# Kernel optimization log

Hardware: AMD Instinct MI355X
Metric: run time of the kernel (lower is better)

Reference implementation:

```python
import jax, jax.numpy as jnp
import numpy as np

N_NODES = 100000
N_EDGES = 1600000
IN_F = 64
HIDDEN = [64, 64, 32]


def _glorot(key, shape):
    limit = float(np.sqrt(6.0 / (shape[0] + shape[1])))
    return jax.random.uniform(key, shape, jnp.float32, -limit, limit)


def setup_inputs() -> dict:
    key = jax.random.key(0)
    ks = jax.random.split(key, 5)
    x = jax.random.normal(ks[0], (N_NODES, IN_F), jnp.float32)
    edge_index = jax.random.randint(ks[1], (2, N_EDGES), 0, N_NODES, jnp.int64)
    dims = [IN_F] + HIDDEN
    params = {}
    for i in range(len(HIDDEN)):
        params[f"W{i+1}"] = _glorot(ks[2 + i], (dims[i], dims[i + 1]))
        params[f"b{i+1}"] = jnp.zeros((dims[i + 1],), jnp.float32)
    return {"x": x, "edge_index": edge_index, **params}


def _gcn_layer(x, src, dst, norm, W, b, n):
    # PyG GCNConv: linear transform, then normalized scatter-sum aggregation, then bias
    h = x @ W                                  # [N, out]
    msg = norm[:, None] * h[src]               # gather + edge scaling, [E+N, out]
    out = jax.ops.segment_sum(msg, dst, num_segments=n)
    return out + b


def reference(x, edge_index, W1, b1, W2, b2, W3, b3):
    n = x.shape[0]
    # add self-loops (GCNConv default add_self_loops=True)
    loops = jnp.arange(n, dtype=edge_index.dtype)
    src = jnp.concatenate([edge_index[0], loops])
    dst = jnp.concatenate([edge_index[1], loops])
    # symmetric normalization: deg over destination (col), norm = d^-1/2[src]*d^-1/2[dst]
    deg = jax.ops.segment_sum(jnp.ones_like(src, x.dtype), dst, num_segments=n)
    dinv = jnp.where(deg > 0, jax.lax.rsqrt(deg), 0.0)
    norm = dinv[src] * dinv[dst]
    h = jax.nn.relu(_gcn_layer(x, src, dst, norm, W1, b1, n))
    h = jax.nn.relu(_gcn_layer(h, src, dst, norm, W2, b2, n))
    return _gcn_layer(h, src, dst, norm, W3, b3, n)
```

## Files before the change

### kernel.cpp

```cpp
#include <hip/hip_runtime.h>
#include <hip/hip_bf16.h>


#define BLOCK 256
#define NBUCKET 512
#define CHUNK 4096
#define SLOT 4608
#define MAX_NPB 256

typedef float f32x4 __attribute__((ext_vector_type(4)));
typedef short bf16x8 __attribute__((ext_vector_type(8)));

__device__ __forceinline__ float4 fma4(float s, float4 a, float4 b) {
  return make_float4(fmaf(s, a.x, b.x), fmaf(s, a.y, b.y),
                     fmaf(s, a.z, b.z), fmaf(s, a.w, b.w));
}

__device__ __forceinline__ unsigned int bf16r(float f) {
  unsigned int u = __float_as_uint(f);
  u += 0x7fffu + ((u >> 16) & 1u);
  return u >> 16;
}

__device__ __forceinline__ void bsplit(float v, unsigned int& h,
                                       unsigned int& l) {
  h = bf16r(v);
  float r = v - __uint_as_float(h << 16);
  l = bf16r(r);
}

__device__ __forceinline__ void acc_bf8(float4& lo, float4& hi, uint4 u) {
  lo.x += __uint_as_float(u.x << 16);
  lo.y += __uint_as_float(u.x & 0xffff0000u);
  lo.z += __uint_as_float(u.y << 16);
  lo.w += __uint_as_float(u.y & 0xffff0000u);
  hi.x += __uint_as_float(u.z << 16);
  hi.y += __uint_as_float(u.z & 0xffff0000u);
  hi.z += __uint_as_float(u.w << 16);
  hi.w += __uint_as_float(u.w & 0xffff0000u);
// ... 45 lines not shown
      binned[b2 * SLOT + base[b2] + o2] = s4.z | ((d4.z - b2 * npb) << 17);
      binned[b3 * SLOT + base[b3] + o3] = s4.w | ((d4.w - b3 * npb) << 17);
    } else {
      for (int t = 0; t < 4; ++t) {
        if (i + t < e) {
          int d = dst[i + t];
          int bkt = d / npb;
          int lofs = atomicAdd(&h[bkt], 1);
          binned[bkt * SLOT + base[bkt] + lofs] =
              src[i + t] | ((d - bkt * npb) << 17);
        }
      }
    }
  }
}

__global__ __launch_bounds__(BLOCK) void bucket_build(
    const int* __restrict__ binned, const int* __restrict__ bcursor,
    int* __restrict__ offs, int* __restrict__ cnt, float* __restrict__ dinv,
    int* __restrict__ csr_src, int n, int npb) {
  __shared__ int nhist[MAX_NPB];
  __shared__ int noff[MAX_NPB];
  __shared__ int lcsr[SLOT];
  const int b = blockIdx.x;
  const int node_base = b * npb;
  const int nodes = min(npb, n - node_base);
  if (nodes <= 0) return;
  const int ebase = b * SLOT;
  const int ecnt = bcursor[b];
  for (int i = threadIdx.x; i < npb; i += BLOCK) nhist[i] = 0;
  __syncthreads();
  for (int i = threadIdx.x; i < ecnt; i += BLOCK)
    atomicAdd(&nhist[binned[ebase + i] >> 17], 1);
  __syncthreads();
  if (threadIdx.x < 64) {
    const int lane = threadIdx.x;
    const int bi = lane * 4;
    int v0 = (bi + 0 < nodes) ? nhist[bi + 0] : 0;
    int v1 = (bi + 1 < nodes) ? nhist[bi + 1] : 0;
    int v2 = (bi + 2 < nodes) ? nhist[bi + 2] : 0;
    int v3 = (bi + 3 < nodes) ? nhist[bi + 3] : 0;
    int tsum = v0 + v1 + v2 + v3;
    int s = tsum;
#pragma unroll
    for (int o = 1; o < 64; o <<= 1) {
      int u = __shfl_up(s, o, 64);
      if (lane >= o) s += u;
    }
    int texcl = s - tsum;
    if (bi + 0 < nodes) noff[bi + 0] = texcl;
    if (bi + 1 < nodes) noff[bi + 1] = texcl + v0;
    if (bi + 2 < nodes) noff[bi + 2] = texcl + v0 + v1;
    if (bi + 3 < nodes) noff[bi + 3] = texcl + v0 + v1 + v2;
  }
  __syncthreads();
  for (int i = threadIdx.x; i < nodes; i += BLOCK) {
    int c = nhist[i];
    offs[node_base + i] = ebase + noff[i];
    cnt[node_base + i] = c;
    dinv[node_base + i] = rsqrtf((float)(c + 1));
  }
  __syncthreads();
  for (int i = threadIdx.x; i < ecnt; i += BLOCK) {
    int v = binned[ebase + i];
    int pos = atomicAdd(&noff[v >> 17], 1);
    lcsr[pos] = v & 0x1ffff;
  }
  __syncthreads();
  for (int i = threadIdx.x; i < ecnt; i += BLOCK)
    csr_src[ebase + i] = lcsr[i];
}

__global__ __launch_bounds__(BLOCK) void wprep_kernel(
    const float* __restrict__ W1, const float* __restrict__ W2,
    const float* __restrict__ W3, unsigned short* __restrict__ Wt) {
  int t = blockIdx.x * BLOCK + threadIdx.x;
  float v;
  int hi_off, lo_off;
  if (t < 4096) {
    int nn = t >> 6, k = t & 63;
    v = W1[k * 64 + nn];
    hi_off = t;
    lo_off = 4096 + t;
  } else if (t < 8192) {
    int i = t - 4096;
    int nn = i >> 6, k = i & 63;
    v = W2[k * 64 + nn];
    hi_off = 8192 + i;
    lo_off = 12288 + i;
  } else {
    int i = t - 8192;
    if (i >= 2048) return;
    int nn = i >> 6, k = i & 63;
    v = W3[k * 32 + nn];
    hi_off = 16384 + i;
    lo_off = 18432 + i;
  }
  unsigned int h, l;
  bsplit(v, h, l);
  Wt[hi_off] = (unsigned short)h;
  Wt[lo_off] = (unsigned short)l;
}


__global__ __launch_bounds__(BLOCK) void gemm1_kernel(
    const float* __restrict__ x, const unsigned short* __restrict__ Wt,
    const float* __restrict__ dinv, unsigned short* __restrict__ hbf, int n) {
  __shared__ unsigned short Ahi[16][72];
  __shared__ unsigned short Alo[16][72];
  __shared__ float dvs[16];
  const int r16 = threadIdx.x >> 4;
  const int c4 = (threadIdx.x & 15) * 4;
  const int node = blockIdx.x * 16 + r16;
  const int wv = threadIdx.x >> 6;
  const int fr = threadIdx.x & 15;
  const int fq = (threadIdx.x >> 4) & 3;
  const unsigned short* wb = Wt + ((wv * 16 + fr) * 64) + fq * 8;
  bf16x8 bh0 = *(const bf16x8*)(wb);
  bf16x8 bh1 = *(const bf16x8*)(wb + 32);
  bf16x8 bl0 = *(const bf16x8*)(wb + 4096);
  bf16x8 bl1 = *(const bf16x8*)(wb + 4096 + 32);
  uint2 ph = make_uint2(0u, 0u), pl = make_uint2(0u, 0u);
  if (node < n) {
    f32x4 xv =
        __builtin_nontemporal_load((const f32x4*)(x + (size_t)node * 64 + c4));
    unsigned int h0, l0, h1, l1, h2, l2, h3, l3;
    bsplit(xv.x, h0, l0);
    bsplit(xv.y, h1, l1);
    bsplit(xv.z, h2, l2);
    bsplit(xv.w, h3, l3);
    ph = make_uint2(h0 | (h1 << 16), h2 | (h3 << 16));
    pl = make_uint2(l0 | (l1 << 16), l2 | (l3 << 16));
  }
  *(uint2*)(&Ahi[r16][c4]) = ph;
  *(uint2*)(&Alo[r16][c4]) = pl;
  if ((threadIdx.x & 15) == 0) dvs[r16] = (node < n) ? dinv[node] : 0.f;
  __syncthreads();
  bf16x8 ah0 = *(const bf16x8*)(&Ahi[fr][fq * 8]);
  bf16x8 ah1 = *(const bf16x8*)(&Ahi[fr][fq * 8 + 32]);
  bf16x8 aL0 = *(const bf16x8*)(&Alo[fr][fq * 8]);
  bf16x8 aL1 = *(const bf16x8*)(&Alo[fr][fq * 8 + 32]);
  f32x4 acc = {0.f, 0.f, 0.f, 0.f};
  acc = __builtin_amdgcn_mfma_f32_16x16x32_bf16(ah0, bh0, acc, 0, 0, 0);
  acc = __builtin_amdgcn_mfma_f32_16x16x32_bf16(aL0, bh0, acc, 0, 0, 0);
  acc = __builtin_amdgcn_mfma_f32_16x16x32_bf16(ah0, bl0, acc, 0, 0, 0);
  acc = __builtin_amdgcn_mfma_f32_16x16x32_bf16(ah1, bh1, acc, 0, 0, 0);
  acc = __builtin_amdgcn_mfma_f32_16x16x32_bf16(aL1, bh1, acc, 0, 0, 0);
  acc = __builtin_amdgcn_mfma_f32_16x16x32_bf16(ah1, bl1, acc, 0, 0, 0);
  const int col = wv * 16 + fr;
#pragma unroll
  for (int j = 0; j < 4; ++j) {
    int row = fq * 4 + j;
    int nd = blockIdx.x * 16 + row;
    if (nd < n)
      hbf[(size_t)nd * 64 + col] = (unsigned short)bf16r(dvs[row] * acc[j]);
  }
}

__global__ __launch_bounds__(BLOCK) void fused_agg_gemm64(
    const unsigned short* __restrict__ hin, const int* __restrict__ csr_src,
    const int* __restrict__ offs, const int* __restrict__ cnt,
    const float* __restrict__ dinv, const float* __restrict__ bias,
    const unsigned short* __restrict__ Wt, unsigned short* __restrict__ hout,
    int n) {
  __shared__ unsigned short Ahi[16][72];
  __shared__ unsigned short Alo[16][72];
  __shared__ float dvs[16];
  const int g = threadIdx.x >> 4;
  const int lane16 = threadIdx.x & 15;
  const int colgrp = lane16 & 7;
  const int half = lane16 >> 3;
  const int c8 = colgrp * 8;
  const int node = blockIdx.x * 16 + g;
  const bool valid = node < n;
  float dnode = 0.f;
  uint4 qh = make_uint4(0u, 0u, 0u, 0u), ql = make_uint4(0u, 0u, 0u, 0u);
  if (valid) {
    const int start = offs[node];
    const int cn = cnt[node];
    const unsigned short* hcol = hin + c8;
    float4 l0 = make_float4(0.f, 0.f, 0.f, 0.f), h0 = l0;
    float4 l1 = l0, h1 = l0, l2 = l0, h2 = l0, l3 = l0, h3 = l0;
    if (half == 0)
      acc_bf8(l0, h0, *(const uint4*)(hcol + (size_t)node * 64));
    int j = half * 4;
    for (; j + 4 <= cn; j += 8) {
      int s0 = csr_src[start + j + 0];
      int s1 = csr_src[start + j + 1];
      int s2 = csr_src[start + j + 2];
      int s3 = csr_src[start + j + 3];
      uint4 u0 = *(const uint4*)(hcol + (size_t)s0 * 64);
      uint4 u1 = *(const uint4*)(hcol + (size_t)s1 * 64);
      uint4 u2 = *(const uint4*)(hcol + (size_t)s2 * 64);
      uint4 u3 = *(const uint4*)(hcol + (size_t)s3 * 64);
      acc_bf8(l0, h0, u0);
      acc_bf8(l1, h1, u1);
      acc_bf8(l2, h2, u2);
      acc_bf8(l3, h3, u3);
    }
    if (j < cn) {
      int rem = cn - j;
      int s0 = csr_src[start + j];
      acc_bf8(l1, h1, *(const uint4*)(hcol + (size_t)s0 * 64));
      if (rem > 1) {
        int s1 = csr_src[start + j + 1];
        acc_bf8(l2, h2, *(const uint4*)(hcol + (size_t)s1 * 64));
      }
      if (rem > 2) {
        int s2 = csr_src[start + j + 2];
        acc_bf8(l3, h3, *(const uint4*)(hcol + (size_t)s2 * 64));
      }
    }
    float4 alo = make_float4((l0.x + l1.x) + (l2.x + l3.x),
                             (l0.y + l1.y) + (l2.y + l3.y),
                             (l0.z + l1.z) + (l2.z + l3.z),
                             (l0.w + l1.w) + (l2.w + l3.w));
    float4 ahi = make_float4((h0.x + h1.x) + (h2.x + h3.x),
                             (h0.y + h1.y) + (h2.y + h3.y),
                             (h0.z + h1.z) + (h2.z + h3.z),
                             (h0.w + h1.w) + (h2.w + h3.w));
    alo.x += __shfl_xor(alo.x, 8); alo.y += __shfl_xor(alo.y, 8);
    alo.z += __shfl_xor(alo.z, 8); alo.w += __shfl_xor(alo.w, 8);
    ahi.x += __shfl_xor(ahi.x, 8); ahi.y += __shfl_xor(ahi.y, 8);
    ahi.z += __shfl_xor(ahi.z, 8); ahi.w += __shfl_xor(ahi.w, 8);
    dnode = dinv[node];
    if (half == 0) {
      float4 b4l = *(const float4*)(bias + c8);
      float4 b4h = *(const float4*)(bias + c8 + 4);
      float v0 = fmaxf(fmaf(dnode, alo.x, b4l.x), 0.f);
      float v1 = fmaxf(fmaf(dnode, alo.y, b4l.y), 0.f);
      float v2 = fmaxf(fmaf(dnode, alo.z, b4l.z), 0.f);
      float v3 = fmaxf(fmaf(dnode, alo.w, b4l.w), 0.f);
      float v4 = fmaxf(fmaf(dnode, ahi.x, b4h.x), 0.f);
      float v5 = fmaxf(fmaf(dnode, ahi.y, b4h.y), 0.f);
      float v6 = fmaxf(fmaf(dnode, ahi.z, b4h.z), 0.f);
      float v7 = fmaxf(fmaf(dnode, ahi.w, b4h.w), 0.f);
      unsigned int h0u, l0u, h1u, l1u, h2u, l2u, h3u, l3u;
      unsigned int h4u, l4u, h5u, l5u, h6u, l6u, h7u, l7u;
      bsplit(v0, h0u, l0u); bsplit(v1, h1u, l1u);
      bsplit(v2, h2u, l2u); bsplit(v3, h3u, l3u);
      bsplit(v4, h4u, l4u); bsplit(v5, h5u, l5u);
      bsplit(v6, h6u, l6u); bsplit(v7, h7u, l7u);
      qh = make_uint4(h0u | (h1u << 16), h2u | (h3u << 16),
                      h4u | (h5u << 16), h6u | (h7u << 16));
      ql = make_uint4(l0u | (l1u << 16), l2u | (l3u << 16),
                      l4u | (l5u << 16), l6u | (l7u << 16));
    }
  }
  if (half == 0) {
    *(uint4*)(&Ahi[g][c8]) = qh;
    *(uint4*)(&Alo[g][c8]) = ql;
    if (lane16 == 0) dvs[g] = dnode;
  }
  const int wv = threadIdx.x >> 6;
  const int fr = threadIdx.x & 15;
  const int fq = (threadIdx.x >> 4) & 3;
  const unsigned short* wb = Wt + ((wv * 16 + fr) * 64) + fq * 8;
  bf16x8 bh0 = *(const bf16x8*)(wb);
  bf16x8 bh1 = *(const bf16x8*)(wb + 32);
  bf16x8 bl0 = *(const bf16x8*)(wb + 4096);
  bf16x8 bl1 = *(const bf16x8*)(wb + 4096 + 32);
  __syncthreads();
  bf16x8 ah0 = *(const bf16x8*)(&Ahi[fr][fq * 8]);
  bf16x8 ah1 = *(const bf16x8*)(&Ahi[fr][fq * 8 + 32]);
  bf16x8 aL0 = *(const bf16x8*)(&Alo[fr][fq * 8]);
  bf16x8 aL1 = *(const bf16x8*)(&Alo[fr][fq * 8 + 32]);
  f32x4 acc = {0.f, 0.f, 0.f, 0.f};
  acc = __builtin_amdgcn_mfma_f32_16x16x32_bf16(ah0, bh0, acc, 0, 0, 0);
  acc = __builtin_amdgcn_mfma_f32_16x16x32_bf16(aL0, bh0, acc, 0, 0, 0);
  acc = __builtin_amdgcn_mfma_f32_16x16x32_bf16(ah0, bl0, acc, 0, 0, 0);
  acc = __builtin_amdgcn_mfma_f32_16x16x32_bf16(ah1, bh1, acc, 0, 0, 0);
  acc = __builtin_amdgcn_mfma_f32_16x16x32_bf16(aL1, bh1, acc, 0, 0, 0);
  acc = __builtin_amdgcn_mfma_f32_16x16x32_bf16(ah1, bl1, acc, 0, 0, 0);
  const int col = wv * 16 + fr;
#pragma unroll
  for (int j = 0; j < 4; ++j) {
    int row = fq * 4 + j;
    int nd = blockIdx.x * 16 + row;
    if (nd < n)
      hout[(size_t)nd * 64 + col] = (unsigned short)bf16r(dvs[row] * acc[j]);
  }
}

__global__ __launch_bounds__(BLOCK) void fused_agg_gemm32(
    const unsigned short* __restrict__ hin, const int* __restrict__ csr_src,
    const int* __restrict__ offs, const int* __restrict__ cnt,
    const float* __restrict__ dinv, const float* __restrict__ bias,
    const unsigned short* __restrict__ Wt, unsigned short* __restrict__ hout,
    int n) {
  __shared__ unsigned short Ahi[32][72];
  __shared__ unsigned short Alo[32][72];
  __shared__ float dvs[32];
  const int g = threadIdx.x >> 3;
  const int lane8 = threadIdx.x & 7;
  const int c8 = lane8 * 8;
  const int node = blockIdx.x * 32 + g;
  const bool valid = node < n;
  float dnode = 0.f;
  uint4 qh = make_uint4(0u, 0u, 0u, 0u), ql = make_uint4(0u, 0u, 0u, 0u);
  if (valid) {
    const int start = offs[node];
    const int cn = cnt[node];
    const unsigned short* hcol = hin + c8;
    float4 l0 = make_float4(0.f, 0.f, 0.f, 0.f), h0 = l0;
    float4 l1 = l0, h1 = l0, l2 = l0, h2 = l0, l3 = l0, h3 = l0;
    acc_bf8(l0, h0, *(const uint4*)(hcol + (size_t)node * 64));
    int j = 0;
    for (; j + 4 <= cn; j += 4) {
      int s0 = csr_src[start + j + 0];
      int s1 = csr_src[start + j + 1];
      int s2 = csr_src[start + j + 2];
      int s3 = csr_src[start + j + 3];
      uint4 u0 = *(const uint4*)(hcol + (size_t)s0 * 64);
      uint4 u1 = *(const uint4*)(hcol + (size_t)s1 * 64);
      uint4 u2 = *(const uint4*)(hcol + (size_t)s2 * 64);
      uint4 u3 = *(const uint4*)(hcol + (size_t)s3 * 64);
      acc_bf8(l0, h0, u0);
      acc_bf8(l1, h1, u1);
      acc_bf8(l2, h2, u2);
      acc_bf8(l3, h3, u3);
    }
    if (j + 2 <= cn) {
      int s0 = csr_src[start + j + 0];
      int s1 = csr_src[start + j + 1];
      uint4 u0 = *(const uint4*)(hcol + (size_t)s0 * 64);
      uint4 u1 = *(const uint4*)(hcol + (size_t)s1 * 64);
      acc_bf8(l1, h1, u0);
      acc_bf8(l2, h2, u1);
      j += 2;
    }
    if (j < cn) {
      int s0 = csr_src[start + j];
      acc_bf8(l3, h3, *(const uint4*)(hcol + (size_t)s0 * 64));
    }
    float4 alo = make_float4((l0.x + l1.x) + (l2.x + l3.x),
                             (l0.y + l1.y) + (l2.y + l3.y),
                             (l0.z + l1.z) + (l2.z + l3.z),
                             (l0.w + l1.w) + (l2.w + l3.w));
    float4 ahi = make_float4((h0.x + h1.x) + (h2.x + h3.x),
                             (h0.y + h1.y) + (h2.y + h3.y),
                             (h0.z + h1.z) + (h2.z + h3.z),
                             (h0.w + h1.w) + (h2.w + h3.w));
    dnode = dinv[node];
    float4 b4l = *(const float4*)(bias + c8);
    float4 b4h = *(const float4*)(bias + c8 + 4);
    float v0 = fmaxf(fmaf(dnode, alo.x, b4l.x), 0.f);
    float v1 = fmaxf(fmaf(dnode, alo.y, b4l.y), 0.f);
    float v2 = fmaxf(fmaf(dnode, alo.z, b4l.z), 0.f);
    float v3 = fmaxf(fmaf(dnode, alo.w, b4l.w), 0.f);
    float v4 = fmaxf(fmaf(dnode, ahi.x, b4h.x), 0.f);
    float v5 = fmaxf(fmaf(dnode, ahi.y, b4h.y), 0.f);
    float v6 = fmaxf(fmaf(dnode, ahi.z, b4h.z), 0.f);
    float v7 = fmaxf(fmaf(dnode, ahi.w, b4h.w), 0.f);
    unsigned int h0u, l0u, h1u, l1u, h2u, l2u, h3u, l3u;
    unsigned int h4u, l4u, h5u, l5u, h6u, l6u, h7u, l7u;
    bsplit(v0, h0u, l0u); bsplit(v1, h1u, l1u);
    bsplit(v2, h2u, l2u); bsplit(v3, h3u, l3u);
    bsplit(v4, h4u, l4u); bsplit(v5, h5u, l5u);
    bsplit(v6, h6u, l6u); bsplit(v7, h7u, l7u);
    qh = make_uint4(h0u | (h1u << 16), h2u | (h3u << 16),
                    h4u | (h5u << 16), h6u | (h7u << 16));
    ql = make_uint4(l0u | (l1u << 16), l2u | (l3u << 16),
                    l4u | (l5u << 16), l6u | (l7u << 16));
  }
  *(uint4*)(&Ahi[g][c8]) = qh;
  *(uint4*)(&Alo[g][c8]) = ql;
  if (lane8 == 0) dvs[g] = dnode;
  const int wv = threadIdx.x >> 6;
  const int mt = wv >> 1;
  const int nt = wv & 1;
  const int fr = threadIdx.x & 15;
  const int fq = (threadIdx.x >> 4) & 3;
  const unsigned short* wb = Wt + ((nt * 16 + fr) * 64) + fq * 8;
  bf16x8 bh0 = *(const bf16x8*)(wb);
  bf16x8 bh1 = *(const bf16x8*)(wb + 32);
  bf16x8 bl0 = *(const bf16x8*)(wb + 2048);
  bf16x8 bl1 = *(const bf16x8*)(wb + 2048 + 32);
  __syncthreads();
  bf16x8 ah0 = *(const bf16x8*)(&Ahi[mt * 16 + fr][fq * 8]);
  bf16x8 ah1 = *(const bf16x8*)(&Ahi[mt * 16 + fr][fq * 8 + 32]);
  bf16x8 aL0 = *(const bf16x8*)(&Alo[mt * 16 + fr][fq * 8]);
  bf16x8 aL1 = *(const bf16x8*)(&Alo[mt * 16 + fr][fq * 8 + 32]);
  f32x4 acc = {0.f, 0.f, 0.f, 0.f};
  acc = __builtin_amdgcn_mfma_f32_16x16x32_bf16(ah0, bh0, acc, 0, 0, 0);
  acc = __builtin_amdgcn_mfma_f32_16x16x32_bf16(aL0, bh0, acc, 0, 0, 0);
  acc = __builtin_amdgcn_mfma_f32_16x16x32_bf16(ah0, bl0, acc, 0, 0, 0);
  acc = __builtin_amdgcn_mfma_f32_16x16x32_bf16(ah1, bh1, acc, 0, 0, 0);
  acc = __builtin_amdgcn_mfma_f32_16x16x32_bf16(aL1, bh1, acc, 0, 0, 0);
  acc = __builtin_amdgcn_mfma_f32_16x16x32_bf16(ah1, bl1, acc, 0, 0, 0);
  const int col = nt * 16 + fr;
#pragma unroll
  for (int j = 0; j < 4; ++j) {
    int row = mt * 16 + fq * 4 + j;
    int nd = blockIdx.x * 32 + row;
    if (nd < n)
      hout[(size_t)nd * 32 + col] = (unsigned short)bf16r(dvs[row] * acc[j]);
  }
}

__global__ __launch_bounds__(BLOCK) void agg3_kernel(
    const unsigned short* __restrict__ hbf, const int* __restrict__ csr_src,
    const int* __restrict__ offs, const int* __restrict__ cnt,
    const float* __restrict__ dinv, const float* __restrict__ bias,
    float* __restrict__ out, int n) {
  constexpr int F = 32;
  const int node = blockIdx.x * 64 + (int)(threadIdx.x >> 2);
  const int c8 = (threadIdx.x & 3) * 8;
  if (node >= n) return;
  const int start = offs[node];
  const int cn = cnt[node];
  const unsigned short* hcol = hbf + c8;
  float4 l0 = make_float4(0.f, 0.f, 0.f, 0.f), h0 = l0;
  float4 l1 = l0, h1 = l0, l2 = l0, h2 = l0, l3 = l0, h3 = l0;
  acc_bf8(l0, h0, *(const uint4*)(hcol + (size_t)node * F));
  int j = 0;
  for (; j + 4 <= cn; j += 4) {
    int s0 = csr_src[start + j + 0];
    int s1 = csr_src[start + j + 1];
    int s2 = csr_src[start + j + 2];
    int s3 = csr_src[start + j + 3];
    uint4 u0 = *(const uint4*)(hcol + (size_t)s0 * F);
    uint4 u1 = *(const uint4*)(hcol + (size_t)s1 * F);
    uint4 u2 = *(const uint4*)(hcol + (size_t)s2 * F);
    uint4 u3 = *(const uint4*)(hcol + (size_t)s3 * F);
    acc_bf8(l0, h0, u0);
    acc_bf8(l1, h1, u1);
    acc_bf8(l2, h2, u2);
    acc_bf8(l3, h3, u3);
  }
  if (j + 2 <= cn) {
    int s0 = csr_src[start + j + 0];
    int s1 = csr_src[start + j + 1];
    uint4 u0 = *(const uint4*)(hcol + (size_t)s0 * F);
    uint4 u1 = *(const uint4*)(hcol + (size_t)s1 * F);
    acc_bf8(l1, h1, u0);
    acc_bf8(l2, h2, u1);
    j += 2;
  }
  if (j < cn) {
    int s0 = csr_src[start + j];
    acc_bf8(l3, h3, *(const uint4*)(hcol + (size_t)s0 * F));
  }
  float4 alo = make_float4((l0.x + l1.x) + (l2.x + l3.x),
                           (l0.y + l1.y) + (l2.y + l3.y),
                           (l0.z + l1.z) + (l2.z + l3.z),
                           (l0.w + l1.w) + (l2.w + l3.w));
  float4 ahi = make_float4((h0.x + h1.x) + (h2.x + h3.x),
                           (h0.y + h1.y) + (h2.y + h3.y),
                           (h0.z + h1.z) + (h2.z + h3.z),
                           (h0.w + h1.w) + (h2.w + h3.w));
  float d = dinv[node];
  float4 blo = *(const float4*)(bias + c8);
  float4 bhi = *(const float4*)(bias + c8 + 4);
  f32x4 vlo = {fmaf(d, alo.x, blo.x), fmaf(d, alo.y, blo.y),
               fmaf(d, alo.z, blo.z), fmaf(d, alo.w, blo.w)};
  f32x4 vhi = {fmaf(d, ahi.x, bhi.x), fmaf(d, ahi.y, bhi.y),
               fmaf(d, ahi.z, bhi.z), fmaf(d, ahi.w, bhi.w)};
  float* op = out + (size_t)node * F + c8;
  __builtin_nontemporal_store(vlo, (f32x4*)op);
  __builtin_nontemporal_store(vhi, (f32x4*)(op + 4));
}

static inline size_t align_up(size_t v, size_t a) { return (v + a - 1) & ~(a - 1); }

extern "C" void kernel_launch(void* const* d_in, const int* in_sizes, int n_in,
// ... 23 lines not shown
  float* dinv  = (float*)(ws + off); off = align_up(off + (size_t)n * 4, 512);
  int* binned  = (int*)(ws + off); off = align_up(off + (size_t)NBUCKET * SLOT * 4, 512);
  int* csr_src = (int*)(ws + off); off = align_up(off + (size_t)NBUCKET * SLOT * 4, 512);
  unsigned short* hbuf_a = (unsigned short*)(ws + off);
  off = align_up(off + (size_t)n * 64 * 2, 512);
  unsigned short* hbuf_b = (unsigned short*)(ws + off);
  off = align_up(off + (size_t)n * 64 * 2, 512);
  unsigned short* Wt = (unsigned short*)(ws + off);
  off = align_up(off + (size_t)20480 * 2, 512);
  (void)ws_size;

  unsigned short* Wt1 = Wt;
  unsigned short* Wt2 = Wt + 8192;
  unsigned short* Wt3 = Wt + 16384;

  const int gC = (e + CHUNK - 1) / CHUNK;

  hipMemsetAsync(bcursor, 0, NBUCKET * 4, stream);
  wprep_kernel<<<40, BLOCK, 0, stream>>>(W1, W2, W3, Wt);
  binning_kernel<<<gC, BLOCK, 0, stream>>>(e_src, e_dst, bcursor, binned, e, npb);
  bucket_build<<<NBUCKET, BLOCK, 0, stream>>>(binned, bcursor, offs, cnt, dinv,
                                              csr_src, n, npb);

  gemm1_kernel<<<(n + 15) / 16, BLOCK, 0, stream>>>(x, Wt1, dinv, hbuf_a, n);
  fused_agg_gemm64<<<(n + 15) / 16, BLOCK, 0, stream>>>(
      hbuf_a, csr_src, offs, cnt, dinv, b1, Wt2, hbuf_b, n);
  fused_agg_gemm32<<<(n + 31) / 32, BLOCK, 0, stream>>>(
      hbuf_b, csr_src, offs, cnt, dinv, b2, Wt3, hbuf_a, n);
  agg3_kernel<<<(n + 63) / 64, BLOCK, 0, stream>>>(hbuf_a, csr_src, offs, cnt,
                                                   dinv, b3, out, n);
}
```

Measured before the change: 242.8 us.

## Persistent grid-stride GEMM kernels, padded CSR rows, and vectorized index loads

Converts gemm1 and both fused aggregation+GEMM kernels into persistent grid-stride loops over a fixed 2048-block grid. The weight fragments are loaded once per block, and double-buffered shared tiles avoid a second barrier per tile. Each node's CSR segment is padded to a multiple of four so the neighbor indices can be read as int4 vectors, and 32-bit shift addressing replaces 64-bit multiplies. The padded tails hold stale or uninitialized entries; they are not read because the loops stop at cnt. Padding can overflow SLOT for high-degree buckets, which the code only partly guards with a min on the copy length.

```diff
diff --git a/kernel.cpp b/kernel.cpp
--- a/kernel.cpp
+++ b/kernel.cpp
@@ -7,14 +7,10 @@
 #define CHUNK 4096
 #define SLOT 4608
 #define MAX_NPB 256
+#define PGRID 2048
 
 typedef float f32x4 __attribute__((ext_vector_type(4)));
 typedef short bf16x8 __attribute__((ext_vector_type(8)));
-
-__device__ __forceinline__ float4 fma4(float s, float4 a, float4 b) {
-  return make_float4(fmaf(s, a.x, b.x), fmaf(s, a.y, b.y),
-                     fmaf(s, a.z, b.z), fmaf(s, a.w, b.w));
-}
 
 __device__ __forceinline__ unsigned int bf16r(float f) {
   unsigned int u = __float_as_uint(f);
@@ -106,6 +102,7 @@
   __shared__ int nhist[MAX_NPB];
   __shared__ int noff[MAX_NPB];
   __shared__ int lcsr[SLOT];
+  __shared__ int ptot_sh;
   const int b = blockIdx.x;
   const int node_base = b * npb;
   const int nodes = min(npb, n - node_base);
@@ -124,7 +121,11 @@
     int v1 = (bi + 1 < nodes) ? nhist[bi + 1] : 0;
     int v2 = (bi + 2 < nodes) ? nhist[bi + 2] : 0;
     int v3 = (bi + 3 < nodes) ? nhist[bi + 3] : 0;
-    int tsum = v0 + v1 + v2 + v3;
+    int p0 = (v0 + 3) & ~3;
+    int p1 = (v1 + 3) & ~3;
+    int p2 = (v2 + 3) & ~3;
+    int p3 = (v3 + 3) & ~3;
+    int tsum = p0 + p1 + p2 + p3;
     int s = tsum;
 #pragma unroll
     for (int o = 1; o < 64; o <<= 1) {
@@ -133,11 +134,13 @@
     }
     int texcl = s - tsum;
     if (bi + 0 < nodes) noff[bi + 0] = texcl;
-    if (bi + 1 < nodes) noff[bi + 1] = texcl + v0;
-    if (bi + 2 < nodes) noff[bi + 2] = texcl + v0 + v1;
-    if (bi + 3 < nodes) noff[bi + 3] = texcl + v0 + v1 + v2;
-  }
-  __syncthreads();
+    if (bi + 1 < nodes) noff[bi + 1] = texcl + p0;
+    if (bi + 2 < nodes) noff[bi + 2] = texcl + p0 + p1;
+    if (bi + 3 < nodes) noff[bi + 3] = texcl + p0 + p1 + p2;
+    if (lane == 63) ptot_sh = s;
+  }
+  __syncthreads();
+  const int ptot = min(ptot_sh, SLOT);
   for (int i = threadIdx.x; i < nodes; i += BLOCK) {
     int c = nhist[i];
     offs[node_base + i] = ebase + noff[i];
@@ -151,7 +154,7 @@
     lcsr[pos] = v & 0x1ffff;
   }
   __syncthreads();
-  for (int i = threadIdx.x; i < ecnt; i += BLOCK)
+  for (int i = threadIdx.x; i < ptot; i += BLOCK)
     csr_src[ebase + i] = lcsr[i];
 }
 
@@ -190,12 +193,11 @@
 __global__ __launch_bounds__(BLOCK) void gemm1_kernel(
     const float* __restrict__ x, const unsigned short* __restrict__ Wt,
     const float* __restrict__ dinv, unsigned short* __restrict__ hbf, int n) {
-  __shared__ unsigned short Ahi[16][72];
-  __shared__ unsigned short Alo[16][72];
-  __shared__ float dvs[16];
+  __shared__ unsigned short Ahi[2][16][72];
+  __shared__ unsigned short Alo[2][16][72];
+  __shared__ float dvs[2][16];
   const int r16 = threadIdx.x >> 4;
   const int c4 = (threadIdx.x & 15) * 4;
-  const int node = blockIdx.x * 16 + r16;
   const int wv = threadIdx.x >> 6;
   const int fr = threadIdx.x & 15;
   const int fq = (threadIdx.x >> 4) & 3;
@@ -204,40 +206,46 @@
   bf16x8 bh1 = *(const bf16x8*)(wb + 32);
   bf16x8 bl0 = *(const bf16x8*)(wb + 4096);
   bf16x8 bl1 = *(const bf16x8*)(wb + 4096 + 32);
-  uint2 ph = make_uint2(0u, 0u), pl = make_uint2(0u, 0u);
-  if (node < n) {
-    f32x4 xv =
-        __builtin_nontemporal_load((const f32x4*)(x + (size_t)node * 64 + c4));
-    unsigned int h0, l0, h1, l1, h2, l2, h3, l3;
-    bsplit(xv.x, h0, l0);
-    bsplit(xv.y, h1, l1);
-    bsplit(xv.z, h2, l2);
-    bsplit(xv.w, h3, l3);
-    ph = make_uint2(h0 | (h1 << 16), h2 | (h3 << 16));
-    pl = make_uint2(l0 | (l1 << 16), l2 | (l3 << 16));
-  }
-  *(uint2*)(&Ahi[r16][c4]) = ph;
-  *(uint2*)(&Alo[r16][c4]) = pl;
-  if ((threadIdx.x & 15) == 0) dvs[r16] = (node < n) ? dinv[node] : 0.f;
-  __syncthreads();
-  bf16x8 ah0 = *(const bf16x8*)(&Ahi[fr][fq * 8]);
-  bf16x8 ah1 = *(const bf16x8*)(&Ahi[fr][fq * 8 + 32]);
-  bf16x8 aL0 = *(const bf16x8*)(&Alo[fr][fq * 8]);
-  bf16x8 aL1 = *(const bf16x8*)(&Alo[fr][fq * 8 + 32]);
-  f32x4 acc = {0.f, 0.f, 0.f, 0.f};
-  acc = __builtin_amdgcn_mfma_f32_16x16x32_bf16(ah0, bh0, acc, 0, 0, 0);
-  acc = __builtin_amdgcn_mfma_f32_16x16x32_bf16(aL0, bh0, acc, 0, 0, 0);
-  acc = __builtin_amdgcn_mfma_f32_16x16x32_bf16(ah0, bl0, acc, 0, 0, 0);
-  acc = __builtin_amdgcn_mfma_f32_16x16x32_bf16(ah1, bh1, acc, 0, 0, 0);
-  acc = __builtin_amdgcn_mfma_f32_16x16x32_bf16(aL1, bh1, acc, 0, 0, 0);
-  acc = __builtin_amdgcn_mfma_f32_16x16x32_bf16(ah1, bl1, acc, 0, 0, 0);
-  const int col = wv * 16 + fr;
+  const int ntiles = (n + 15) >> 4;
+  int p = 0;
+  for (int tile = blockIdx.x; tile < ntiles; tile += gridDim.x, p ^= 1) {
+    const int node = tile * 16 + r16;
+    uint2 ph = make_uint2(0u, 0u), pl = make_uint2(0u, 0u);
+    if (node < n) {
+      f32x4 xv = __builtin_nontemporal_load(
+          (const f32x4*)(x + (size_t)node * 64 + c4));
+      unsigned int h0, l0, h1, l1, h2, l2, h3, l3;
+      bsplit(xv.x, h0, l0);
+      bsplit(xv.y, h1, l1);
+      bsplit(xv.z, h2, l2);
+      bsplit(xv.w, h3, l3);
+      ph = make_uint2(h0 | (h1 << 16), h2 | (h3 << 16));
+      pl = make_uint2(l0 | (l1 << 16), l2 | (l3 << 16));
+    }
+    *(uint2*)(&Ahi[p][r16][c4]) = ph;
+    *(uint2*)(&Alo[p][r16][c4]) = pl;
+    if ((threadIdx.x & 15) == 0) dvs[p][r16] = (node < n) ? dinv[node] : 0.f;
+    __syncthreads();
+    bf16x8 ah0 = *(const bf16x8*)(&Ahi[p][fr][fq * 8]);
+    bf16x8 ah1 = *(const bf16x8*)(&Ahi[p][fr][fq * 8 + 32]);
+    bf16x8 aL0 = *(const bf16x8*)(&Alo[p][fr][fq * 8]);
+    bf16x8 aL1 = *(const bf16x8*)(&Alo[p][fr][fq * 8 + 32]);
+    f32x4 acc = {0.f, 0.f, 0.f, 0.f};
+    acc = __builtin_amdgcn_mfma_f32_16x16x32_bf16(ah0, bh0, acc, 0, 0, 0);
+    acc = __builtin_amdgcn_mfma_f32_16x16x32_bf16(aL0, bh0, acc, 0, 0, 0);
+    acc = __builtin_amdgcn_mfma_f32_16x16x32_bf16(ah0, bl0, acc, 0, 0, 0);
+    acc = __builtin_amdgcn_mfma_f32_16x16x32_bf16(ah1, bh1, acc, 0, 0, 0);
+    acc = __builtin_amdgcn_mfma_f32_16x16x32_bf16(aL1, bh1, acc, 0, 0, 0);
+    acc = __builtin_amdgcn_mfma_f32_16x16x32_bf16(ah1, bl1, acc, 0, 0, 0);
+    const int col = wv * 16 + fr;
 #pragma unroll
-  for (int j = 0; j < 4; ++j) {
-    int row = fq * 4 + j;
-    int nd = blockIdx.x * 16 + row;
-    if (nd < n)
-      hbf[(size_t)nd * 64 + col] = (unsigned short)bf16r(dvs[row] * acc[j]);
+    for (int j = 0; j < 4; ++j) {
+      int row = fq * 4 + j;
+      int nd = tile * 16 + row;
+      if (nd < n)
+        hbf[(size_t)nd * 64 + col] =
+            (unsigned short)bf16r(dvs[p][row] * acc[j]);
+    }
   }
 }
 
@@ -247,68 +255,191 @@
     const float* __restrict__ dinv, const float* __restrict__ bias,
     const unsigned short* __restrict__ Wt, unsigned short* __restrict__ hout,
     int n) {
-  __shared__ unsigned short Ahi[16][72];
-  __shared__ unsigned short Alo[16][72];
-  __shared__ float dvs[16];
+  __shared__ unsigned short Ahi[2][16][72];
+  __shared__ unsigned short Alo[2][16][72];
+  __shared__ float dvs[2][16];
   const int g = threadIdx.x >> 4;
   const int lane16 = threadIdx.x & 15;
   const int colgrp = lane16 & 7;
   const int half = lane16 >> 3;
   const int c8 = colgrp * 8;
-  const int node = blockIdx.x * 16 + g;
-  const bool valid = node < n;
-  float dnode = 0.f;
-  uint4 qh = make_uint4(0u, 0u, 0u, 0u), ql = make_uint4(0u, 0u, 0u, 0u);
-  if (valid) {
-    const int start = offs[node];
-    const int cn = cnt[node];
-    const unsigned short* hcol = hin + c8;
-    float4 l0 = make_float4(0.f, 0.f, 0.f, 0.f), h0 = l0;
-    float4 l1 = l0, h1 = l0, l2 = l0, h2 = l0, l3 = l0, h3 = l0;
-    if (half == 0)
-      acc_bf8(l0, h0, *(const uint4*)(hcol + (size_t)node * 64));
-    int j = half * 4;
-    for (; j + 4 <= cn; j += 8) {
-      int s0 = csr_src[start + j + 0];
-      int s1 = csr_src[start + j + 1];
-      int s2 = csr_src[start + j + 2];
-      int s3 = csr_src[start + j + 3];
-      uint4 u0 = *(const uint4*)(hcol + (size_t)s0 * 64);
-      uint4 u1 = *(const uint4*)(hcol + (size_t)s1 * 64);
-      uint4 u2 = *(const uint4*)(hcol + (size_t)s2 * 64);
-      uint4 u3 = *(const uint4*)(hcol + (size_t)s3 * 64);
-      acc_bf8(l0, h0, u0);
-      acc_bf8(l1, h1, u1);
-      acc_bf8(l2, h2, u2);
-      acc_bf8(l3, h3, u3);
-    }
-    if (j < cn) {
-      int rem = cn - j;
-      int s0 = csr_src[start + j];
-      acc_bf8(l1, h1, *(const uint4*)(hcol + (size_t)s0 * 64));
-      if (rem > 1) {
-        int s1 = csr_src[start + j + 1];
-        acc_bf8(l2, h2, *(const uint4*)(hcol + (size_t)s1 * 64));
+  const int wv = threadIdx.x >> 6;
+  const int fr = threadIdx.x & 15;
+  const int fq = (threadIdx.x >> 4) & 3;
+  const unsigned short* wb = Wt + ((wv * 16 + fr) * 64) + fq * 8;
+  bf16x8 bh0 = *(const bf16x8*)(wb);
+  bf16x8 bh1 = *(const bf16x8*)(wb + 32);
+  bf16x8 bl0 = *(const bf16x8*)(wb + 4096);
+  bf16x8 bl1 = *(const bf16x8*)(wb + 4096 + 32);
+  const char* hbase = (const char*)hin + c8 * 2;
+  const int ntiles = (n + 15) >> 4;
+  int p = 0;
+  for (int tile = blockIdx.x; tile < ntiles; tile += gridDim.x, p ^= 1) {
+    const int node = tile * 16 + g;
+    const bool valid = node < n;
+    float dnode = 0.f;
+    uint4 qh = make_uint4(0u, 0u, 0u, 0u), ql = make_uint4(0u, 0u, 0u, 0u);
+    if (valid) {
+      const int start = offs[node];
+      const int cn = cnt[node];
+      const int* cp = csr_src + start;
+      float4 l0 = make_float4(0.f, 0.f, 0.f, 0.f), h0 = l0;
+      float4 l1 = l0, h1 = l0, l2 = l0, h2 = l0, l3 = l0, h3 = l0;
+      if (half == 0)
+        acc_bf8(l0, h0,
+                *(const uint4*)(hbase + ((unsigned)node << 7)));
+      int j = half * 4;
+      for (; j + 4 <= cn; j += 8) {
+        int4 sv = *(const int4*)(cp + j);
+        uint4 u0 = *(const uint4*)(hbase + ((unsigned)sv.x << 7));
+        uint4 u1 = *(const uint4*)(hbase + ((unsigned)sv.y << 7));
+        uint4 u2 = *(const uint4*)(hbase + ((unsigned)sv.z << 7));
+        uint4 u3 = *(const uint4*)(hbase + ((unsigned)sv.w << 7));
+        acc_bf8(l0, h0, u0);
+        acc_bf8(l1, h1, u1);
+        acc_bf8(l2, h2, u2);
+        acc_bf8(l3, h3, u3);
       }
-      if (rem > 2) {
-        int s2 = csr_src[start + j + 2];
-        acc_bf8(l3, h3, *(const uint4*)(hcol + (size_t)s2 * 64));
+      if (j < cn) {
+        int rem = cn - j;
+        acc_bf8(l1, h1, *(const uint4*)(hbase + ((unsigned)cp[j] << 7)));
+        if (rem > 1)
+          acc_bf8(l2, h2, *(const uint4*)(hbase + ((unsigned)cp[j + 1] << 7)));
+        if (rem > 2)
+          acc_bf8(l3, h3, *(const uint4*)(hbase + ((unsigned)cp[j + 2] << 7)));
       }
-    }
-    float4 alo = make_float4((l0.x + l1.x) + (l2.x + l3.x),
-                             (l0.y + l1.y) + (l2.y + l3.y),
-                             (l0.z + l1.z) + (l2.z + l3.z),
-                             (l0.w + l1.w) + (l2.w + l3.w));
-    float4 ahi = make_float4((h0.x + h1.x) + (h2.x + h3.x),
-                             (h0.y + h1.y) + (h2.y + h3.y),
-                             (h0.z + h1.z) + (h2.z + h3.z),
-                             (h0.w + h1.w) + (h2.w + h3.w));
-    alo.x += __shfl_xor(alo.x, 8); alo.y += __shfl_xor(alo.y, 8);
-    alo.z += __shfl_xor(alo.z, 8); alo.w += __shfl_xor(alo.w, 8);
-    ahi.x += __shfl_xor(ahi.x, 8); ahi.y += __shfl_xor(ahi.y, 8);
-    ahi.z += __shfl_xor(ahi.z, 8); ahi.w += __shfl_xor(ahi.w, 8);
-    dnode = dinv[node];
+      float4 alo = make_float4((l0.x + l1.x) + (l2.x + l3.x),
+                               (l0.y + l1.y) + (l2.y + l3.y),
+                               (l0.z + l1.z) + (l2.z + l3.z),
+                               (l0.w + l1.w) + (l2.w + l3.w));
+      float4 ahi = make_float4((h0.x + h1.x) + (h2.x + h3.x),
+                               (h0.y + h1.y) + (h2.y + h3.y),
+                               (h0.z + h1.z) + (h2.z + h3.z),
+                               (h0.w + h1.w) + (h2.w + h3.w));
+      alo.x += __shfl_xor(alo.x, 8); alo.y += __shfl_xor(alo.y, 8);
+      alo.z += __shfl_xor(alo.z, 8); alo.w += __shfl_xor(alo.w, 8);
+      ahi.x += __shfl_xor(ahi.x, 8); ahi.y += __shfl_xor(ahi.y, 8);
+      ahi.z += __shfl_xor(ahi.z, 8); ahi.w += __shfl_xor(ahi.w, 8);
+      dnode = dinv[node];
+      if (half == 0) {
+        float4 b4l = *(const float4*)(bias + c8);
+        float4 b4h = *(const float4*)(bias + c8 + 4);
+        float v0 = fmaxf(fmaf(dnode, alo.x, b4l.x), 0.f);
+        float v1 = fmaxf(fmaf(dnode, alo.y, b4l.y), 0.f);
+        float v2 = fmaxf(fmaf(dnode, alo.z, b4l.z), 0.f);
+        float v3 = fmaxf(fmaf(dnode, alo.w, b4l.w), 0.f);
+        float v4 = fmaxf(fmaf(dnode, ahi.x, b4h.x), 0.f);
+        float v5 = fmaxf(fmaf(dnode, ahi.y, b4h.y), 0.f);
+        float v6 = fmaxf(fmaf(dnode, ahi.z, b4h.z), 0.f);
+        float v7 = fmaxf(fmaf(dnode, ahi.w, b4h.w), 0.f);
+        unsigned int h0u, l0u, h1u, l1u, h2u, l2u, h3u, l3u;
+        unsigned int h4u, l4u, h5u, l5u, h6u, l6u, h7u, l7u;
+        bsplit(v0, h0u, l0u); bsplit(v1, h1u, l1u);
+        bsplit(v2, h2u, l2u); bsplit(v3, h3u, l3u);
+        bsplit(v4, h4u, l4u); bsplit(v5, h5u, l5u);
+        bsplit(v6, h6u, l6u); bsplit(v7, h7u, l7u);
+        qh = make_uint4(h0u | (h1u << 16), h2u | (h3u << 16),
+                        h4u | (h5u << 16), h6u | (h7u << 16));
+        ql = make_uint4(l0u | (l1u << 16), l2u | (l3u << 16),
+                        l4u | (l5u << 16), l6u | (l7u << 16));
+      }
+    }
     if (half == 0) {
+      *(uint4*)(&Ahi[p][g][c8]) = qh;
+      *(uint4*)(&Alo[p][g][c8]) = ql;
+      if (lane16 == 0) dvs[p][g] = dnode;
+    }
+    __syncthreads();
+    bf16x8 ah0 = *(const bf16x8*)(&Ahi[p][fr][fq * 8]);
+    bf16x8 ah1 = *(const bf16x8*)(&Ahi[p][fr][fq * 8 + 32]);
+    bf16x8 aL0 = *(const bf16x8*)(&Alo[p][fr][fq * 8]);
+    bf16x8 aL1 = *(const bf16x8*)(&Alo[p][fr][fq * 8 + 32]);
+    f32x4 acc = {0.f, 0.f, 0.f, 0.f};
+    acc = __builtin_amdgcn_mfma_f32_16x16x32_bf16(ah0, bh0, acc, 0, 0, 0);
+    acc = __builtin_amdgcn_mfma_f32_16x16x32_bf16(aL0, bh0, acc, 0, 0, 0);
+    acc = __builtin_amdgcn_mfma_f32_16x16x32_bf16(ah0, bl0, acc, 0, 0, 0);
+    acc = __builtin_amdgcn_mfma_f32_16x16x32_bf16(ah1, bh1, acc, 0, 0, 0);
+    acc = __builtin_amdgcn_mfma_f32_16x16x32_bf16(aL1, bh1, acc, 0, 0, 0);
+    acc = __builtin_amdgcn_mfma_f32_16x16x32_bf16(ah1, bl1, acc, 0, 0, 0);
+    const int col = wv * 16 + fr;
+#pragma unroll
+    for (int j = 0; j < 4; ++j) {
+      int row = fq * 4 + j;
+      int nd = tile * 16 + row;
+      if (nd < n)
+        hout[(size_t)nd * 64 + col] =
+            (unsigned short)bf16r(dvs[p][row] * acc[j]);
+    }
+  }
+}
+
+__global__ __launch_bounds__(BLOCK) void fused_agg_gemm32(
+    const unsigned short* __restrict__ hin, const int* __restrict__ csr_src,
+    const int* __restrict__ offs, const int* __restrict__ cnt,
+    const float* __restrict__ dinv, const float* __restrict__ bias,
+    const unsigned short* __restrict__ Wt, unsigned short* __restrict__ hout,
+    int n) {
+  __shared__ unsigned short Ahi[2][32][72];
+  __shared__ unsigned short Alo[2][32][72];
+  __shared__ float dvs[2][32];
+  const int g = threadIdx.x >> 3;
+  const int lane8 = threadIdx.x & 7;
+  const int c8 = lane8 * 8;
+  const int wv = threadIdx.x >> 6;
+  const int mt = wv >> 1;
+  const int nt = wv & 1;
+  const int fr = threadIdx.x & 15;
+  const int fq = (threadIdx.x >> 4) & 3;
+  const unsigned short* wb = Wt + ((nt * 16 + fr) * 64) + fq * 8;
+  bf16x8 bh0 = *(const bf16x8*)(wb);
+  bf16x8 bh1 = *(const bf16x8*)(wb + 32);
+  bf16x8 bl0 = *(const bf16x8*)(wb + 2048);
+  bf16x8 bl1 = *(const bf16x8*)(wb + 2048 + 32);
+  const char* hbase = (const char*)hin + c8 * 2;
+  const int ntiles = (n + 31) >> 5;
+  int p = 0;
+  for (int tile = blockIdx.x; tile < ntiles; tile += gridDim.x, p ^= 1) {
+    const int node = tile * 32 + g;
+    const bool valid = node < n;
+    float dnode = 0.f;
+    uint4 qh = make_uint4(0u, 0u, 0u, 0u), ql = make_uint4(0u, 0u, 0u, 0u);
+    if (valid) {
+      const int start = offs[node];
+      const int cn = cnt[node];
+      const int* cp = csr_src + start;
+      float4 l0 = make_float4(0.f, 0.f, 0.f, 0.f), h0 = l0;
+      float4 l1 = l0, h1 = l0, l2 = l0, h2 = l0, l3 = l0, h3 = l0;
+      acc_bf8(l0, h0, *(const uint4*)(hbase + ((unsigned)node << 7)));
+      int j = 0;
+      for (; j + 4 <= cn; j += 4) {
+        int4 sv = *(const int4*)(cp + j);
+        uint4 u0 = *(const uint4*)(hbase + ((unsigned)sv.x << 7));
+        uint4 u1 = *(const uint4*)(hbase + ((unsigned)sv.y << 7));
+        uint4 u2 = *(const uint4*)(hbase + ((unsigned)sv.z << 7));
+        uint4 u3 = *(const uint4*)(hbase + ((unsigned)sv.w << 7));
+        acc_bf8(l0, h0, u0);
+        acc_bf8(l1, h1, u1);
+        acc_bf8(l2, h2, u2);
+        acc_bf8(l3, h3, u3);
+      }
+      if (j + 2 <= cn) {
+        uint4 u0 = *(const uint4*)(hbase + ((unsigned)cp[j] << 7));
+        uint4 u1 = *(const uint4*)(hbase + ((unsigned)cp[j + 1] << 7));
+        acc_bf8(l1, h1, u0);
+        acc_bf8(l2, h2, u1);
+        j += 2;
+      }
+      if (j < cn)
+        acc_bf8(l3, h3, *(const uint4*)(hbase + ((unsigned)cp[j] << 7)));
+      float4 alo = make_float4((l0.x + l1.x) + (l2.x + l3.x),
+                               (l0.y + l1.y) + (l2.y + l3.y),
+                               (l0.z + l1.z) + (l2.z + l3.z),
+                               (l0.w + l1.w) + (l2.w + l3.w));
+      float4 ahi = make_float4((h0.x + h1.x) + (h2.x + h3.x),
+                               (h0.y + h1.y) + (h2.y + h3.y),
+                               (h0.z + h1.z) + (h2.z + h3.z),
+                               (h0.w + h1.w) + (h2.w + h3.w));
+      dnode = dinv[node];
       float4 b4l = *(const float4*)(bias + c8);
       float4 b4h = *(const float4*)(bias + c8 + 4);
       float v0 = fmaxf(fmaf(dnode, alo.x, b4l.x), 0.f);
@@ -330,155 +461,30 @@
       ql = make_uint4(l0u | (l1u << 16), l2u | (l3u << 16),
                       l4u | (l5u << 16), l6u | (l7u << 16));
     }
-  }
-  if (half == 0) {
-    *(uint4*)(&Ahi[g][c8]) = qh;
-    *(uint4*)(&Alo[g][c8]) = ql;
-    if (lane16 == 0) dvs[g] = dnode;
-  }
-  const int wv = threadIdx.x >> 6;
-  const int fr = threadIdx.x & 15;
-  const int fq = (threadIdx.x >> 4) & 3;
-  const unsigned short* wb = Wt + ((wv * 16 + fr) * 64) + fq * 8;
-  bf16x8 bh0 = *(const bf16x8*)(wb);
-  bf16x8 bh1 = *(const bf16x8*)(wb + 32);
-  bf16x8 bl0 = *(const bf16x8*)(wb + 4096);
-  bf16x8 bl1 = *(const bf16x8*)(wb + 4096 + 32);
-  __syncthreads();
-  bf16x8 ah0 = *(const bf16x8*)(&Ahi[fr][fq * 8]);
-  bf16x8 ah1 = *(const bf16x8*)(&Ahi[fr][fq * 8 + 32]);
-  bf16x8 aL0 = *(const bf16x8*)(&Alo[fr][fq * 8]);
-  bf16x8 aL1 = *(const bf16x8*)(&Alo[fr][fq * 8 + 32]);
-  f32x4 acc = {0.f, 0.f, 0.f, 0.f};
-  acc = __builtin_amdgcn_mfma_f32_16x16x32_bf16(ah0, bh0, acc, 0, 0, 0);
-  acc = __builtin_amdgcn_mfma_f32_16x16x32_bf16(aL0, bh0, acc, 0, 0, 0);
-  acc = __builtin_amdgcn_mfma_f32_16x16x32_bf16(ah0, bl0, acc, 0, 0, 0);
-  acc = __builtin_amdgcn_mfma_f32_16x16x32_bf16(ah1, bh1, acc, 0, 0, 0);
-  acc = __builtin_amdgcn_mfma_f32_16x16x32_bf16(aL1, bh1, acc, 0, 0, 0);
-  acc = __builtin_amdgcn_mfma_f32_16x16x32_bf16(ah1, bl1, acc, 0, 0, 0);
-  const int col = wv * 16 + fr;
+    *(uint4*)(&Ahi[p][g][c8]) = qh;
+    *(uint4*)(&Alo[p][g][c8]) = ql;
+    if (lane8 == 0) dvs[p][g] = dnode;
+    __syncthreads();
+    bf16x8 ah0 = *(const bf16x8*)(&Ahi[p][mt * 16 + fr][fq * 8]);
+    bf16x8 ah1 = *(const bf16x8*)(&Ahi[p][mt * 16 + fr][fq * 8 + 32]);
+    bf16x8 aL0 = *(const bf16x8*)(&Alo[p][mt * 16 + fr][fq * 8]);
+    bf16x8 aL1 = *(const bf16x8*)(&Alo[p][mt * 16 + fr][fq * 8 + 32]);
+    f32x4 acc = {0.f, 0.f, 0.f, 0.f};
+    acc = __builtin_amdgcn_mfma_f32_16x16x32_bf16(ah0, bh0, acc, 0, 0, 0);
+    acc = __builtin_amdgcn_mfma_f32_16x16x32_bf16(aL0, bh0, acc, 0, 0, 0);
+    acc = __builtin_amdgcn_mfma_f32_16x16x32_bf16(ah0, bl0, acc, 0, 0, 0);
+    acc = __builtin_amdgcn_mfma_f32_16x16x32_bf16(ah1, bh1, acc, 0, 0, 0);
+    acc = __builtin_amdgcn_mfma_f32_16x16x32_bf16(aL1, bh1, acc, 0, 0, 0);
+    acc = __builtin_amdgcn_mfma_f32_16x16x32_bf16(ah1, bl1, acc, 0, 0, 0);
+    const int col = nt * 16 + fr;
 #pragma unroll
-  for (int j = 0; j < 4; ++j) {
-    int row = fq * 4 + j;
-    int nd = blockIdx.x * 16 + row;
-    if (nd < n)
-      hout[(size_t)nd * 64 + col] = (unsigned short)bf16r(dvs[row] * acc[j]);
-  }
-}
-
-__global__ __launch_bounds__(BLOCK) void fused_agg_gemm32(
-    const unsigned short* __restrict__ hin, const int* __restrict__ csr_src,
-    const int* __restrict__ offs, const int* __restrict__ cnt,
-    const float* __restrict__ dinv, const float* __restrict__ bias,
-    const unsigned short* __restrict__ Wt, unsigned short* __restrict__ hout,
-    int n) {
-  __shared__ unsigned short Ahi[32][72];
-  __shared__ unsigned short Alo[32][72];
-  __shared__ float dvs[32];
-  const int g = threadIdx.x >> 3;
-  const int lane8 = threadIdx.x & 7;
-  const int c8 = lane8 * 8;
-  const int node = blockIdx.x * 32 + g;
-  const bool valid = node < n;
-  float dnode = 0.f;
-  uint4 qh = make_uint4(0u, 0u, 0u, 0u), ql = make_uint4(0u, 0u, 0u, 0u);
-  if (valid) {
-    const int start = offs[node];
-    const int cn = cnt[node];
-    const unsigned short* hcol = hin + c8;
-    float4 l0 = make_float4(0.f, 0.f, 0.f, 0.f), h0 = l0;
-    float4 l1 = l0, h1 = l0, l2 = l0, h2 = l0, l3 = l0, h3 = l0;
-    acc_bf8(l0, h0, *(const uint4*)(hcol + (size_t)node * 64));
-    int j = 0;
-    for (; j + 4 <= cn; j += 4) {
-      int s0 = csr_src[start + j + 0];
-      int s1 = csr_src[start + j + 1];
-      int s2 = csr_src[start + j + 2];
-      int s3 = csr_src[start + j + 3];
-      uint4 u0 = *(const uint4*)(hcol + (size_t)s0 * 64);
-      uint4 u1 = *(const uint4*)(hcol + (size_t)s1 * 64);
-      uint4 u2 = *(const uint4*)(hcol + (size_t)s2 * 64);
-      uint4 u3 = *(const uint4*)(hcol + (size_t)s3 * 64);
-      acc_bf8(l0, h0, u0);
-      acc_bf8(l1, h1, u1);
-      acc_bf8(l2, h2, u2);
-      acc_bf8(l3, h3, u3);
-    }
-    if (j + 2 <= cn) {
-      int s0 = csr_src[start + j + 0];
-      int s1 = csr_src[start + j + 1];
-      uint4 u0 = *(const uint4*)(hcol + (size_t)s0 * 64);
-      uint4 u1 = *(const uint4*)(hcol + (size_t)s1 * 64);
-      acc_bf8(l1, h1, u0);
-      acc_bf8(l2, h2, u1);
-      j += 2;
-    }
-    if (j < cn) {
-      int s0 = csr_src[start + j];
-      acc_bf8(l3, h3, *(const uint4*)(hcol + (size_t)s0 * 64));
-    }
-    float4 alo = make_float4((l0.x + l1.x) + (l2.x + l3.x),
-                             (l0.y + l1.y) + (l2.y + l3.y),
-                             (l0.z + l1.z) + (l2.z + l3.z),
-                             (l0.w + l1.w) + (l2.w + l3.w));
-    float4 ahi = make_float4((h0.x + h1.x) + (h2.x + h3.x),
-                             (h0.y + h1.y) + (h2.y + h3.y),
-                             (h0.z + h1.z) + (h2.z + h3.z),
-                             (h0.w + h1.w) + (h2.w + h3.w));
-    dnode = dinv[node];
-    float4 b4l = *(const float4*)(bias + c8);
-    float4 b4h = *(const float4*)(bias + c8 + 4);
-    float v0 = fmaxf(fmaf(dnode, alo.x, b4l.x), 0.f);
-    float v1 = fmaxf(fmaf(dnode, alo.y, b4l.y), 0.f);
-    float v2 = fmaxf(fmaf(dnode, alo.z, b4l.z), 0.f);
-    float v3 = fmaxf(fmaf(dnode, alo.w, b4l.w), 0.f);
-    float v4 = fmaxf(fmaf(dnode, ahi.x, b4h.x), 0.f);
-    float v5 = fmaxf(fmaf(dnode, ahi.y, b4h.y), 0.f);
-    float v6 = fmaxf(fmaf(dnode, ahi.z, b4h.z), 0.f);
-    float v7 = fmaxf(fmaf(dnode, ahi.w, b4h.w), 0.f);
-    unsigned int h0u, l0u, h1u, l1u, h2u, l2u, h3u, l3u;
-    unsigned int h4u, l4u, h5u, l5u, h6u, l6u, h7u, l7u;
-    bsplit(v0, h0u, l0u); bsplit(v1, h1u, l1u);
-    bsplit(v2, h2u, l2u); bsplit(v3, h3u, l3u);
-    bsplit(v4, h4u, l4u); bsplit(v5, h5u, l5u);
-    bsplit(v6, h6u, l6u); bsplit(v7, h7u, l7u);
-    qh = make_uint4(h0u | (h1u << 16), h2u | (h3u << 16),
-                    h4u | (h5u << 16), h6u | (h7u << 16));
-    ql = make_uint4(l0u | (l1u << 16), l2u | (l3u << 16),
-                    l4u | (l5u << 16), l6u | (l7u << 16));
-  }
-  *(uint4*)(&Ahi[g][c8]) = qh;
-  *(uint4*)(&Alo[g][c8]) = ql;
-  if (lane8 == 0) dvs[g] = dnode;
-  const int wv = threadIdx.x >> 6;
-  const int mt = wv >> 1;
-  const int nt = wv & 1;
-  const int fr = threadIdx.x & 15;
-  const int fq = (threadIdx.x >> 4) & 3;
-  const unsigned short* wb = Wt + ((nt * 16 + fr) * 64) + fq * 8;
-  bf16x8 bh0 = *(const bf16x8*)(wb);
-  bf16x8 bh1 = *(const bf16x8*)(wb + 32);
-  bf16x8 bl0 = *(const bf16x8*)(wb + 2048);
-  bf16x8 bl1 = *(const bf16x8*)(wb + 2048 + 32);
-  __syncthreads();
-  bf16x8 ah0 = *(const bf16x8*)(&Ahi[mt * 16 + fr][fq * 8]);
-  bf16x8 ah1 = *(const bf16x8*)(&Ahi[mt * 16 + fr][fq * 8 + 32]);
-  bf16x8 aL0 = *(const bf16x8*)(&Alo[mt * 16 + fr][fq * 8]);
-  bf16x8 aL1 = *(const bf16x8*)(&Alo[mt * 16 + fr][fq * 8 + 32]);
-  f32x4 acc = {0.f, 0.f, 0.f, 0.f};
-  acc = __builtin_amdgcn_mfma_f32_16x16x32_bf16(ah0, bh0, acc, 0, 0, 0);
-  acc = __builtin_amdgcn_mfma_f32_16x16x32_bf16(aL0, bh0, acc, 0, 0, 0);
-  acc = __builtin_amdgcn_mfma_f32_16x16x32_bf16(ah0, bl0, acc, 0, 0, 0);
-  acc = __builtin_amdgcn_mfma_f32_16x16x32_bf16(ah1, bh1, acc, 0, 0, 0);
-  acc = __builtin_amdgcn_mfma_f32_16x16x32_bf16(aL1, bh1, acc, 0, 0, 0);
-  acc = __builtin_amdgcn_mfma_f32_16x16x32_bf16(ah1, bl1, acc, 0, 0, 0);
-  const int col = nt * 16 + fr;
-#pragma unroll
-  for (int j = 0; j < 4; ++j) {
-    int row = mt * 16 + fq * 4 + j;
-    int nd = blockIdx.x * 32 + row;
-    if (nd < n)
-      hout[(size_t)nd * 32 + col] = (unsigned short)bf16r(dvs[row] * acc[j]);
+    for (int j = 0; j < 4; ++j) {
+      int row = mt * 16 + fq * 4 + j;
+      int nd = tile * 32 + row;
+      if (nd < n)
+        hout[(size_t)nd * 32 + col] =
+            (unsigned short)bf16r(dvs[p][row] * acc[j]);
+    }
   }
 }
 
@@ -493,38 +499,32 @@
   if (node >= n) return;
   const int start = offs[node];
   const int cn = cnt[node];
-  const unsigned short* hcol = hbf + c8;
+  const int* cp = csr_src + start;
+  const char* hbase = (const char*)hbf + c8 * 2;
   float4 l0 = make_float4(0.f, 0.f, 0.f, 0.f), h0 = l0;
   float4 l1 = l0, h1 = l0, l2 = l0, h2 = l0, l3 = l0, h3 = l0;
-  acc_bf8(l0, h0, *(const uint4*)(hcol + (size_t)node * F));
+  acc_bf8(l0, h0, *(const uint4*)(hbase + ((unsigned)node << 6)));
   int j = 0;
   for (; j + 4 <= cn; j += 4) {
-    int s0 = csr_src[start + j + 0];
-    int s1 = csr_src[start + j + 1];
-    int s2 = csr_src[start + j + 2];
-    int s3 = csr_src[start + j + 3];
-    uint4 u0 = *(const uint4*)(hcol + (size_t)s0 * F);
-    uint4 u1 = *(const uint4*)(hcol + (size_t)s1 * F);
-    uint4 u2 = *(const uint4*)(hcol + (size_t)s2 * F);
-    uint4 u3 = *(const uint4*)(hcol + (size_t)s3 * F);
+    int4 sv = *(const int4*)(cp + j);
+    uint4 u0 = *(const uint4*)(hbase + ((unsigned)sv.x << 6));
+    uint4 u1 = *(const uint4*)(hbase + ((unsigned)sv.y << 6));
+    uint4 u2 = *(const uint4*)(hbase + ((unsigned)sv.z << 6));
+    uint4 u3 = *(const uint4*)(hbase + ((unsigned)sv.w << 6));
     acc_bf8(l0, h0, u0);
     acc_bf8(l1, h1, u1);
     acc_bf8(l2, h2, u2);
     acc_bf8(l3, h3, u3);
   }
   if (j + 2 <= cn) {
-    int s0 = csr_src[start + j + 0];
-    int s1 = csr_src[start + j + 1];
-    uint4 u0 = *(const uint4*)(hcol + (size_t)s0 * F);
-    uint4 u1 = *(const uint4*)(hcol + (size_t)s1 * F);
+    uint4 u0 = *(const uint4*)(hbase + ((unsigned)cp[j] << 6));
+    uint4 u1 = *(const uint4*)(hbase + ((unsigned)cp[j + 1] << 6));
     acc_bf8(l1, h1, u0);
     acc_bf8(l2, h2, u1);
     j += 2;
   }
-  if (j < cn) {
-    int s0 = csr_src[start + j];
-    acc_bf8(l3, h3, *(const uint4*)(hcol + (size_t)s0 * F));
-  }
+  if (j < cn)
+    acc_bf8(l3, h3, *(const uint4*)(hbase + ((unsigned)cp[j] << 6)));
   float4 alo = make_float4((l0.x + l1.x) + (l2.x + l3.x),
                            (l0.y + l1.y) + (l2.y + l3.y),
                            (l0.z + l1.z) + (l2.z + l3.z),
@@ -594,10 +594,10 @@
   bucket_build<<<NBUCKET, BLOCK, 0, stream>>>(binned, bcursor, offs, cnt, dinv,
                                               csr_src, n, npb);
 
-  gemm1_kernel<<<(n + 15) / 16, BLOCK, 0, stream>>>(x, Wt1, dinv, hbuf_a, n);
-  fused_agg_gemm64<<<(n + 15) / 16, BLOCK, 0, stream>>>(
+  gemm1_kernel<<<PGRID, BLOCK, 0, stream>>>(x, Wt1, dinv, hbuf_a, n);
+  fused_agg_gemm64<<<PGRID, BLOCK, 0, stream>>>(
       hbuf_a, csr_src, offs, cnt, dinv, b1, Wt2, hbuf_b, n);
-  fused_agg_gemm32<<<(n + 31) / 32, BLOCK, 0, stream>>>(
+  fused_agg_gemm32<<<PGRID, BLOCK, 0, stream>>>(
       hbuf_b, csr_src, offs, cnt, dinv, b2, Wt3, hbuf_a, n);
   agg3_kernel<<<(n + 63) / 64, BLOCK, 0, stream>>>(hbuf_a, csr_src, offs, cnt,
                                                    dinv, b3, out, n);
```

Measured after the change: 241.1 us. About the same (-0.7%).
